# Kernel tuning notes

Measured on AMD Instinct MI355X. Metric: run time of the kernel, lower is better.

Reference implementation:

```python
import jax, jax.numpy as jnp
import numpy as np

N_NODES = 100000
N_EDGES = 1600000  # undirected edges (each pair listed once, no self loops)
IN_CH, HID, OUT_CH = 512, 64, 32
MU, P, K = 0.1, 1.5, 2
EPS = 1e-8


def setup_inputs() -> dict:
    key = jax.random.key(0)
    k_x, k_src, k_off, k_w1, k_w2 = jax.random.split(key, 5)
    x = jax.random.normal(k_x, (N_NODES, IN_CH), dtype=jnp.float32)
    # undirected edge list with no self loops: dst = (src + offset) % N, offset in [1, N)
    src = jax.random.randint(k_src, (N_EDGES,), 0, N_NODES)
    off = jax.random.randint(k_off, (N_EDGES,), 1, N_NODES)
    dst = (src + off) % N_NODES
    edge_index = jnp.stack([src, dst], axis=0)
    # parameters (lin1 of pGNNNet, lin1 of pGNNConv)
    W1 = jax.random.normal(k_w1, (IN_CH, HID), dtype=jnp.float32) / np.sqrt(IN_CH)
    b1 = jnp.zeros((HID,), dtype=jnp.float32)
    W2 = jax.random.normal(k_w2, (HID, OUT_CH), dtype=jnp.float32) / np.sqrt(HID)
    b2 = jnp.zeros((OUT_CH,), dtype=jnp.float32)
    return {"x": x, "edge_index": edge_index, "W1": W1, "b1": b1, "W2": W2, "b2": b2}


def reference(x, edge_index, W1, b1, W2, b2):
    src, dst = edge_index[0], edge_index[1]
    n = x.shape[0]
    # pGNNNet.lin1 + ReLU (dropout is identity in eval mode)
    h = jax.nn.relu(x @ W1 + b1)                   # [N, HID]
    # pGNNConv.lin1 applied before propagation
    f = h @ W2 + b2                                # [N, OUT]
    # degrees of the symmetric adjacency (no self loops)
    ones = jnp.ones(src.shape, dtype=f.dtype)
    deg = jax.ops.segment_sum(ones, src, num_segments=n) + \
          jax.ops.segment_sum(ones, dst, num_segments=n)
    dinv = jnp.where(deg > 0, 1.0 / deg, 0.0)      # [N]
    dis = jnp.sqrt(dinv)                           # D^{-1/2}
    out = f
    for _ in range(K):
        gs = out * dis[:, None]                    # D^{-1/2} f
        g = gs[src] - gs[dst]                      # graph gradient per edge [E, OUT]
        # edge reweighting: ||grad||^{p-2}
        w = jnp.power(jnp.sum(g * g, axis=1) + EPS, (P - 2.0) * 0.5)   # [E]
        # row sums of M (symmetric, M_ij = w_e)
        s = jax.ops.segment_sum(w, src, num_segments=n) + \
            jax.ops.segment_sum(w, dst, num_segments=n)
        alpha = 1.0 / (s * dinv + MU)              # [N]
        beta = MU * alpha
        # (D^{-1/2} M D^{-1/2} out): scatter-add messages both directions
        m = w[:, None]
        agg = jax.ops.segment_sum(m * gs[dst], src, num_segments=n) + \
              jax.ops.segment_sum(m * gs[src], dst, num_segments=n)
        out = alpha[:, None] * (dis[:, None] * agg) + beta[:, None] * f
    return jax.nn.log_softmax(out, axis=1)
```

## Files before the change

kernel.cpp:

```cpp
#include <hip/hip_runtime.h>
#include <hip/hip_bf16.h>
#include <math.h>

#define N_NODES 100000
#define N_EDGES 1600000
#define IN_CH 512
#define HID 64
#define OUT_CH 32
#define MU 0.1f
#define EPS 1e-8f

#define HE (2 * N_EDGES)
#define ABLK 625
#define EPT 20
#define NBUCK 391
#define BCAP 9216
#define PCAP 10240

typedef short bf16x8 __attribute__((ext_vector_type(8)));
typedef unsigned short us8 __attribute__((ext_vector_type(8)));
typedef float f32x4 __attribute__((ext_vector_type(4)));

__device__ __forceinline__ short f2bf(float f) {
  __hip_bfloat16 h = __float2bfloat16(f);
  return *reinterpret_cast<short*>(&h);
}
__device__ __forceinline__ float bf2f(unsigned short u) {
  unsigned int b = ((unsigned int)u) << 16;
  return __uint_as_float(b);
}

__global__ __launch_bounds__(256) void k_scatter(
    const int* __restrict__ ends, const float* __restrict__ W1,
    const float* __restrict__ W2, short* __restrict__ w1t,
    short* __restrict__ w2t, int* __restrict__ gcur, int* __restrict__ pairs) {
  const int t = threadIdx.x;
  const int b = blockIdx.x;
  {
    const int i = b * 256 + t;
    if (i < IN_CH * HID) {
      int k = i / HID, c = i % HID;
      w1t[c * IN_CH + k] = f2bf(W1[i]);
    } else if (i < IN_CH * HID + HID * OUT_CH) {
      int j = i - IN_CH * HID;
      w2t[(j % OUT_CH) * HID + (j / OUT_CH)] = f2bf(W2[j]);
    }
  }
  __shared__ int cnt[NBUCK];
  for (int i = t; i < NBUCK; i += 256) cnt[i] = 0;
  __syncthreads();
  const int base = b * (256 * EPT);
  int us[EPT];
  #pragma unroll
  for (int j = 0; j < EPT; ++j) us[j] = ends[base + j * 256 + t];
  #pragma unroll
  for (int j = 0; j < EPT; ++j) atomicAdd(&cnt[us[j] >> 8], 1);
  __syncthreads();
  for (int i = t; i < NBUCK; i += 256) {
    const int c = cnt[i];
    cnt[i] = c > 0 ? i * BCAP + atomicAdd(&gcur[i], c) : 0;
  }
  __syncthreads();
  #pragma unroll
  for (int j = 0; j < EPT; ++j) {
    const int i = base + j * 256 + t;
    const int u = us[j];
    const int nb = ends[i < N_EDGES ? i + N_EDGES : i - N_EDGES];
    pairs[atomicAdd(&cnt[u >> 8], 1)] = ((u & 255) << 24) | nb;
  }
}

__global__ __launch_bounds__(256) void k_csr(const int* __restrict__ pairs,
                                             const int* __restrict__ gcur,
                                             int2* __restrict__ degrs,
                                             int* __restrict__ adj) {
  __shared__ int pl[PCAP];
  __shared__ int cnt[256];
  __shared__ int sh[256];
  const int b = blockIdx.x, t = threadIdx.x;
  const int pbase = b * BCAP;
  const int psz = gcur[b];
  const bool fits = psz <= PCAP;
  cnt[t] = 0;
  __syncthreads();
  if (fits) {
    for (int i = t; i < psz; i += 256) {
      int p = pairs[pbase + i];
      pl[i] = p;
      atomicAdd(&cnt[((unsigned)p) >> 24], 1);
    }
  } else {
    for (int i = t; i < psz; i += 256)
      atomicAdd(&cnt[((unsigned)pairs[pbase + i]) >> 24], 1);
  }
  __syncthreads();
  const int d = cnt[t];
  sh[t] = d;
  __syncthreads();
  for (int s = 1; s < 256; s <<= 1) {
    int a = t >= s ? sh[t - s] : 0;
    __syncthreads();
    sh[t] += a;
    __syncthreads();
  }
  const int rs = pbase + sh[t] - d;
  const int v = (b << 8) + t;
  if (v < N_NODES) degrs[v] = make_int2(d, rs);
  __syncthreads();
  cnt[t] = rs;
  __syncthreads();
  for (int i = t; i < psz; i += 256) {
    const int p = fits ? pl[i] : pairs[pbase + i];
    adj[atomicAdd(&cnt[((unsigned)p) >> 24], 1)] = p & 0xFFFFFF;
  }
}

__global__ __launch_bounds__(256, 3) void k_mlp(
    const float* __restrict__ x, const short* __restrict__ w1t,
    const float* __restrict__ b1, const short* __restrict__ w2t,
    const float* __restrict__ b2, const int2* __restrict__ degrs,
    float* __restrict__ f, unsigned short* __restrict__ gs) {
  __shared__ short ht[4][16][72];

  const int t = threadIdx.x;
  const int w = t >> 6;
  const int l = t & 63;
  const int lr = l & 15;
  const int kq = l >> 4;

  const int band = blockIdx.x * 64 + w * 16;
  const int gr = band + lr;
  const int grl = gr < N_NODES ? gr : N_NODES - 1;
  const float* xrow = x + (size_t)grl * IN_CH + kq * 8;

  f32x4 xa[16];
  #pragma unroll
  for (int s = 0; s < 8; ++s) {
    xa[2 * s] = *(const f32x4*)(xrow + s * 32);
    xa[2 * s + 1] = *(const f32x4*)(xrow + s * 32 + 4);
  }
  bf16x8 af[8];
  #pragma unroll
  for (int s = 0; s < 8; ++s) {
    af[s][0] = f2bf(xa[2 * s][0]); af[s][1] = f2bf(xa[2 * s][1]);
    af[s][2] = f2bf(xa[2 * s][2]); af[s][3] = f2bf(xa[2 * s][3]);
    af[s][4] = f2bf(xa[2 * s + 1][0]); af[s][5] = f2bf(xa[2 * s + 1][1]);
    af[s][6] = f2bf(xa[2 * s + 1][2]); af[s][7] = f2bf(xa[2 * s + 1][3]);
  }
  #pragma unroll
  for (int s = 0; s < 8; ++s) {
    xa[2 * s] = *(const f32x4*)(xrow + (s + 8) * 32);
    xa[2 * s + 1] = *(const f32x4*)(xrow + (s + 8) * 32 + 4);
  }
  f32x4 acc1[4] = {};
  #pragma unroll
  for (int s = 0; s < 8; ++s) {
    #pragma unroll
    for (int ct = 0; ct < 4; ++ct) {
      const int c = ct * 16 + lr;
      bf16x8 bfrag = *(const bf16x8*)&w1t[c * IN_CH + s * 32 + kq * 8];
      acc1[ct] = __builtin_amdgcn_mfma_f32_16x16x32_bf16(af[s], bfrag, acc1[ct], 0, 0, 0);
    }
  }
  #pragma unroll
  for (int s = 0; s < 8; ++s) {
    bf16x8 a;
    a[0] = f2bf(xa[2 * s][0]); a[1] = f2bf(xa[2 * s][1]);
    a[2] = f2bf(xa[2 * s][2]); a[3] = f2bf(xa[2 * s][3]);
    a[4] = f2bf(xa[2 * s + 1][0]); a[5] = f2bf(xa[2 * s + 1][1]);
    a[6] = f2bf(xa[2 * s + 1][2]); a[7] = f2bf(xa[2 * s + 1][3]);
    #pragma unroll
    for (int ct = 0; ct < 4; ++ct) {
      const int c = ct * 16 + lr;
      bf16x8 bfrag = *(const bf16x8*)&w1t[c * IN_CH + (s + 8) * 32 + kq * 8];
      acc1[ct] = __builtin_amdgcn_mfma_f32_16x16x32_bf16(a, bfrag, acc1[ct], 0, 0, 0);
    }
  }

  #pragma unroll
  for (int ct = 0; ct < 4; ++ct) {
    const int c = ct * 16 + lr;
    const float bb = b1[c];
    #pragma unroll
    for (int r = 0; r < 4; ++r) {
      float h = acc1[ct][r] + bb;
      ht[w][kq * 4 + r][c] = f2bf(h > 0.f ? h : 0.f);
    }
  }
  __syncthreads();

  f32x4 acc2[2] = {};
  #pragma unroll
  for (int ks = 0; ks < 2; ++ks) {
    bf16x8 a2 = *(const bf16x8*)&ht[w][lr][ks * 32 + kq * 8];
    #pragma unroll
    for (int ct = 0; ct < 2; ++ct) {
      const int c = ct * 16 + lr;
      bf16x8 bfrag = *(const bf16x8*)&w2t[c * HID + ks * 32 + kq * 8];
      acc2[ct] = __builtin_amdgcn_mfma_f32_16x16x32_bf16(a2, bfrag, acc2[ct], 0, 0, 0);
    }
  }

  #pragma unroll
  for (int r = 0; r < 4; ++r) {
    const int gr2 = band + kq * 4 + r;
    if (gr2 < N_NODES) {
      const int d = degrs[gr2].x;
      const float di = d > 0 ? 1.0f / (float)d : 0.0f;
      const float disv = sqrtf(di);
      #pragma unroll
      for (int ct = 0; ct < 2; ++ct) {
        const int c = ct * 16 + lr;
        const float fv = acc2[ct][r] + b2[c];
        f[(size_t)gr2 * OUT_CH + c] = fv;
        gs[(size_t)gr2 * OUT_CH + c] = (unsigned short)f2bf(fv * disv);
      }
    }
  }
}

template <bool FINAL>
__global__ __launch_bounds__(256) void k_prop(
    const unsigned short* __restrict__ gs_in, const float* __restrict__ f,
    const int2* __restrict__ degrs, const int* __restrict__ adj,
    float* __restrict__ outf, unsigned short* __restrict__ outg) {
  const int v = blockIdx.x * 4 + (threadIdx.x >> 6);
  const int lane = threadIdx.x & 63;
  const int slot = lane >> 2;
  const int cg2 = (lane & 3) << 3;

  const int2 dr = degrs[v];
  const int dg = dr.x;
  const int i0 = dr.y;
  const us8 gvu = *(const us8*)&gs_in[v * OUT_CH + cg2];
  const float4 fv0 = *(const float4*)&f[v * OUT_CH + cg2];
  const float4 fv1 = *(const float4*)&f[v * OUT_CH + cg2 + 4];
  float gv[8];
  #pragma unroll
  for (int j = 0; j < 8; ++j) gv[j] = bf2f(gvu[j]);

  const float dinvv = dg > 0 ? 1.0f / (float)dg : 0.0f;
  const float disv = sqrtf(dinvv);

  float accs = 0.f;
  float acca[8] = {0.f, 0.f, 0.f, 0.f, 0.f, 0.f, 0.f, 0.f};

  int u[3];
  #pragma unroll
  for (int q = 0; q < 3; ++q) {
    const int idx = q * 16 + slot;
    u[q] = idx < dg ? adj[i0 + idx] : v;
  }
  us8 guu[3];
  #pragma unroll
  for (int q = 0; q < 3; ++q)
    guu[q] = *(const us8*)&gs_in[u[q] * OUT_CH + cg2];
  #pragma unroll
  for (int q = 0; q < 3; ++q) {
    const bool vq = (q * 16 + slot) < dg;
    float gu[8];
    #pragma unroll
    for (int j = 0; j < 8; ++j) gu[j] = bf2f(guu[q][j]);
    float d = gv[0] - gu[0];
    float sq = d * d;
    #pragma unroll
    for (int j = 1; j < 8; ++j) { d = gv[j] - gu[j]; sq = fmaf(d, d, sq); }
    sq += __shfl_xor(sq, 1);
    sq += __shfl_xor(sq, 2);
    const float wq = vq ? __frsqrt_rn(sqrtf(sq + EPS)) : 0.f;
    accs += wq;
    #pragma unroll
    for (int j = 0; j < 8; ++j) acca[j] = fmaf(wq, gu[j], acca[j]);
  }
  for (int base = 48; base < dg; base += 16) {
    const int idx = base + slot;
    const bool vq = idx < dg;
    const int ut = vq ? adj[i0 + idx] : v;
    const us8 gut = *(const us8*)&gs_in[ut * OUT_CH + cg2];
    float gu[8];
    #pragma unroll
    for (int j = 0; j < 8; ++j) gu[j] = bf2f(gut[j]);
    float d = gv[0] - gu[0];
    float sq = d * d;
    #pragma unroll
    for (int j = 1; j < 8; ++j) { d = gv[j] - gu[j]; sq = fmaf(d, d, sq); }
    sq += __shfl_xor(sq, 1);
    sq += __shfl_xor(sq, 2);
    const float wq = vq ? __frsqrt_rn(sqrtf(sq + EPS)) : 0.f;
    accs += wq;
    #pragma unroll
    for (int j = 0; j < 8; ++j) acca[j] = fmaf(wq, gu[j], acca[j]);
  }

  #pragma unroll
  for (int s = 4; s <= 32; s <<= 1) {
    accs += __shfl_xor(accs, s);
    #pragma unroll
    for (int j = 0; j < 8; ++j) acca[j] += __shfl_xor(acca[j], s);
  }

  const float alpha = 1.0f / (accs * dinvv + MU);
  const float ad = alpha * disv;
  const float ba = MU * alpha;
  float r[8];
  r[0] = fmaf(ad, acca[0], ba * fv0.x);
  r[1] = fmaf(ad, acca[1], ba * fv0.y);
  r[2] = fmaf(ad, acca[2], ba * fv0.z);
  r[3] = fmaf(ad, acca[3], ba * fv0.w);
  r[4] = fmaf(ad, acca[4], ba * fv1.x);
  r[5] = fmaf(ad, acca[5], ba * fv1.y);
  r[6] = fmaf(ad, acca[6], ba * fv1.z);
  r[7] = fmaf(ad, acca[7], ba * fv1.w);

  if (FINAL) {
    float m = r[0];
    #pragma unroll
    for (int j = 1; j < 8; ++j) m = fmaxf(m, r[j]);
    m = fmaxf(m, __shfl_xor(m, 1));
    m = fmaxf(m, __shfl_xor(m, 2));
    float se = 0.f;
    #pragma unroll
    for (int j = 0; j < 8; ++j) se += __expf(r[j] - m);
    se += __shfl_xor(se, 1);
    se += __shfl_xor(se, 2);
    const float lse = m + __logf(se);
    if (slot == 0) {
      float4 o0 = make_float4(r[0] - lse, r[1] - lse, r[2] - lse, r[3] - lse);
      float4 o1 = make_float4(r[4] - lse, r[5] - lse, r[6] - lse, r[7] - lse);
      *(float4*)&outf[v * OUT_CH + cg2] = o0;
      *(float4*)&outf[v * OUT_CH + cg2 + 4] = o1;
    }
  } else {
    if (slot == 0) {
      us8 o;
      #pragma unroll
      for (int j = 0; j < 8; ++j) o[j] = (unsigned short)f2bf(r[j] * disv);
      *(us8*)&outg[v * OUT_CH + cg2] = o;
    }
  }
}

extern "C" void kernel_launch(void* const* d_in, const int* in_sizes, int n_in,
                              void* d_out, int out_size, void* d_ws, size_t ws_size,
                              hipStream_t stream) {
  const float* x = (const float*)d_in[0];
  const int* ei = (const int*)d_in[1];
  const float* W1 = (const float*)d_in[2];
  const float* b1 = (const float*)d_in[3];
  const float* W2 = (const float*)d_in[4];
  const float* b2 = (const float*)d_in[5];
  float* out = (float*)d_out;

  float* f = (float*)d_ws;
  unsigned short* gsa = (unsigned short*)(f + (size_t)N_NODES * 32);
  unsigned short* gsb = gsa + (size_t)N_NODES * 32;
  int2* degrs = (int2*)(gsb + (size_t)N_NODES * 32);
  int* adj = (int*)(degrs + N_NODES);
  short* w1t = (short*)(adj + NBUCK * BCAP);
  short* w2t = w1t + IN_CH * HID;
  int* gcur = (int*)(w2t + HID * OUT_CH);
  int* pairs = (int*)f;

  hipMemsetAsync(gcur, 0, NBUCK * sizeof(int), stream);
  k_scatter<<<ABLK, 256, 0, stream>>>(ei, W1, W2, w1t, w2t, gcur, pairs);
  k_csr<<<NBUCK, 256, 0, stream>>>(pairs, gcur, degrs, adj);
  k_mlp<<<(N_NODES + 63) / 64, 256, 0, stream>>>(x, w1t, b1, w2t, b2, degrs, f, gsa);
  k_prop<false><<<N_NODES / 4, 256, 0, stream>>>(gsa, f, degrs, adj, nullptr, gsb);
  k_prop<true><<<N_NODES / 4, 256, 0, stream>>>(gsb, f, degrs, adj, out, nullptr);
}
```

Baseline: 264.0 us.

## Stage x rows through LDS via global_load_lds in the MLP kernel

Replaces the per-lane register loads of x rows (16 float4 registers held across two halves) with direct global-to-LDS loads into a per-wave staging buffer, processed in four 128-column chunks. Each chunk is waited on with vmcnt(0) and then read back from LDS to build bf16 MFMA fragments. The aim is fully coalesced loads and lower register pressure (the launch-bounds occupancy hint is dropped). In exchange it adds about 33KB of LDS per block and a serialized load-then-compute per chunk with no double buffering, which may expose memory latency.

```diff
diff --git a/kernel.cpp b/kernel.cpp
--- a/kernel.cpp
+++ b/kernel.cpp
@@ -115,65 +115,55 @@
   }
 }
 
-__global__ __launch_bounds__(256, 3) void k_mlp(
+__global__ __launch_bounds__(256) void k_mlp(
     const float* __restrict__ x, const short* __restrict__ w1t,
     const float* __restrict__ b1, const short* __restrict__ w2t,
     const float* __restrict__ b2, const int2* __restrict__ degrs,
     float* __restrict__ f, unsigned short* __restrict__ gs) {
   __shared__ short ht[4][16][72];
+  __shared__ __align__(16) float xstage[4][2080];
 
   const int t = threadIdx.x;
   const int w = t >> 6;
   const int l = t & 63;
   const int lr = l & 15;
   const int kq = l >> 4;
-
   const int band = blockIdx.x * 64 + w * 16;
-  const int gr = band + lr;
-  const int grl = gr < N_NODES ? gr : N_NODES - 1;
-  const float* xrow = x + (size_t)grl * IN_CH + kq * 8;
-
-  f32x4 xa[16];
-  #pragma unroll
-  for (int s = 0; s < 8; ++s) {
-    xa[2 * s] = *(const f32x4*)(xrow + s * 32);
-    xa[2 * s + 1] = *(const f32x4*)(xrow + s * 32 + 4);
-  }
-  bf16x8 af[8];
-  #pragma unroll
-  for (int s = 0; s < 8; ++s) {
-    af[s][0] = f2bf(xa[2 * s][0]); af[s][1] = f2bf(xa[2 * s][1]);
-    af[s][2] = f2bf(xa[2 * s][2]); af[s][3] = f2bf(xa[2 * s][3]);
-    af[s][4] = f2bf(xa[2 * s + 1][0]); af[s][5] = f2bf(xa[2 * s + 1][1]);
-    af[s][6] = f2bf(xa[2 * s + 1][2]); af[s][7] = f2bf(xa[2 * s + 1][3]);
-  }
-  #pragma unroll
-  for (int s = 0; s < 8; ++s) {
-    xa[2 * s] = *(const f32x4*)(xrow + (s + 8) * 32);
-    xa[2 * s + 1] = *(const f32x4*)(xrow + (s + 8) * 32 + 4);
-  }
+
+  float* xb = xstage[w];
+  const int srow = l >> 5;
+  const int sgran = l & 31;
+
   f32x4 acc1[4] = {};
-  #pragma unroll
-  for (int s = 0; s < 8; ++s) {
-    #pragma unroll
-    for (int ct = 0; ct < 4; ++ct) {
-      const int c = ct * 16 + lr;
-      bf16x8 bfrag = *(const bf16x8*)&w1t[c * IN_CH + s * 32 + kq * 8];
-      acc1[ct] = __builtin_amdgcn_mfma_f32_16x16x32_bf16(af[s], bfrag, acc1[ct], 0, 0, 0);
-    }
-  }
-  #pragma unroll
-  for (int s = 0; s < 8; ++s) {
-    bf16x8 a;
-    a[0] = f2bf(xa[2 * s][0]); a[1] = f2bf(xa[2 * s][1]);
-    a[2] = f2bf(xa[2 * s][2]); a[3] = f2bf(xa[2 * s][3]);
-    a[4] = f2bf(xa[2 * s + 1][0]); a[5] = f2bf(xa[2 * s + 1][1]);
-    a[6] = f2bf(xa[2 * s + 1][2]); a[7] = f2bf(xa[2 * s + 1][3]);
-    #pragma unroll
-    for (int ct = 0; ct < 4; ++ct) {
-      const int c = ct * 16 + lr;
-      bf16x8 bfrag = *(const bf16x8*)&w1t[c * IN_CH + (s + 8) * 32 + kq * 8];
-      acc1[ct] = __builtin_amdgcn_mfma_f32_16x16x32_bf16(a, bfrag, acc1[ct], 0, 0, 0);
+  const char* fb = (const char*)xb + (lr >> 1) * 1040 + (lr & 1) * 512 + kq * 32;
+
+  for (int c = 0; c < 4; ++c) {
+    asm volatile("" ::: "memory");
+    #pragma unroll
+    for (int i = 0; i < 8; ++i) {
+      int grow = band + 2 * i + srow;
+      grow = grow < N_NODES ? grow : N_NODES - 1;
+      const float* gsrc = x + (size_t)grow * IN_CH + c * 128 + sgran * 4;
+      __builtin_amdgcn_global_load_lds(
+          (const __attribute__((address_space(1))) void*)gsrc,
+          (__attribute__((address_space(3))) void*)(xb + i * 260),
+          16, 0, 0);
+    }
+    asm volatile("s_waitcnt vmcnt(0)" ::: "memory");
+    #pragma unroll
+    for (int ksub = 0; ksub < 4; ++ksub) {
+      const f32x4 alo = *(const f32x4*)(fb + ksub * 128);
+      const f32x4 ahi = *(const f32x4*)(fb + ksub * 128 + 16);
+      bf16x8 a;
+      a[0] = f2bf(alo[0]); a[1] = f2bf(alo[1]); a[2] = f2bf(alo[2]); a[3] = f2bf(alo[3]);
+      a[4] = f2bf(ahi[0]); a[5] = f2bf(ahi[1]); a[6] = f2bf(ahi[2]); a[7] = f2bf(ahi[3]);
+      const int kg = c * 4 + ksub;
+      #pragma unroll
+      for (int ct = 0; ct < 4; ++ct) {
+        const int cc = ct * 16 + lr;
+        bf16x8 bfrag = *(const bf16x8*)&w1t[cc * IN_CH + kg * 32 + kq * 8];
+        acc1[ct] = __builtin_amdgcn_mfma_f32_16x16x32_bf16(a, bfrag, acc1[ct], 0, 0, 0);
+      }
     }
   }
 
```

Result: faster. 248.0 us (-6.0%).
